# Kernel optimization log

Hardware: AMD Instinct MI355X
Metric: run time of the kernel (lower is better)

Reference implementation:

```python
import math
import jax, jax.numpy as jnp
import numpy as np

B, S, D, H, DH, R, V = 8, 1024, 1024, 8, 512, 36, 32002  # DH = d_model//2, HD = h*DH = 4096
HD = H * DH
LN_EPS = 1e-5


def setup_inputs() -> dict:
    key = jax.random.key(0)
    ks = jax.random.split(key, 16)

    def n(k, shp, std=0.02):
        return jax.random.normal(k, shp, jnp.float32) * std

    pre_words = jax.random.randint(ks[0], (B, S), 0, V)
    img_features = jax.random.normal(ks[1], (B, R, D), jnp.float32)
    exp_embed = n(ks[2], (V, D)).at[0].set(0.0)  # padding_idx=0
    # id2visual table: sparse nonneg rows over 36 regions; zero rows -> textual tokens
    id2vis = (jax.random.uniform(ks[3], (V, R)) < 0.05).astype(jnp.float32)
    # stacked params for 2 transformer layers; weights stored (in, out) so y = x @ W + b
    wq = n(ks[4], (2, D, HD)); bq = jnp.zeros((2, HD), jnp.float32)
    wk = n(ks[5], (2, D, HD)); bk = jnp.zeros((2, HD), jnp.float32)
    wv = n(ks[6], (2, D, HD)); bv = jnp.zeros((2, HD), jnp.float32)
    wo = n(ks[7], (2, HD, D)); bo = jnp.zeros((2, D), jnp.float32)
    w1 = n(ks[8], (2, D, D)); b1 = jnp.zeros((2, D), jnp.float32)
    w2 = n(ks[9], (2, D, D)); b2 = jnp.zeros((2, D), jnp.float32)
    ln1_g = jnp.ones((2, D), jnp.float32); ln1_b = jnp.zeros((2, D), jnp.float32)
    ln2_g = jnp.ones((2, D), jnp.float32); ln2_b = jnp.zeros((2, D), jnp.float32)
    return dict(pre_words=pre_words, img_features=img_features, exp_embed=exp_embed,
                id2vis=id2vis, wq=wq, bq=bq, wk=wk, bk=bk, wv=wv, bv=bv, wo=wo, bo=bo,
                w1=w1, b1=b1, w2=w2, b2=b2, ln1_g=ln1_g, ln1_b=ln1_b, ln2_g=ln2_g, ln2_b=ln2_b)


def _layer_norm(x, g, b):
    m = x.mean(-1, keepdims=True)
    v = ((x - m) ** 2).mean(-1, keepdims=True)
    return (x - m) / jnp.sqrt(v + LN_EPS) * g + b


def _softmax_one(x):
    # shifted-denominator softmax: exp(x - max) / (1 + sum exp(x - max))
    x = x - x.max(-1, keepdims=True)
    e = jnp.exp(x)
    return e / (1.0 + e.sum(-1, keepdims=True))


def reference(pre_words, img_features, exp_embed, id2vis, wq, bq, wk, bk, wv, bv,
              wo, bo, w1, b1, w2, b2, ln1_g, ln1_b, ln2_g, ln2_b):
    # token embedding: textual (masked to 0 where a visual row exists) + visual bmm
    te = exp_embed[pre_words]                       # (B,S,D)
    vids = id2vis[pre_words]                        # (B,S,R)
    word_mask = vids.sum(-1, keepdims=True) != 0    # (B,S,1)
    ve = jnp.einsum('bsr,brd->bsd', vids, img_features)
    x = jnp.where(word_mask, 0.0, te) + ve          # (B,S,D)

    scale = 1.0 / math.sqrt(DH)
    for i in range(2):  # two structurally identical transformer layers
        h = _layer_norm(x, ln1_g[i], ln1_b[i])
        q = (h @ wq[i] + bq[i]).reshape(B, S, H, DH).transpose(0, 2, 1, 3)
        k = (h @ wk[i] + bk[i]).reshape(B, S, H, DH).transpose(0, 2, 1, 3)
        v = (h @ wv[i] + bv[i]).reshape(B, S, H, DH).transpose(0, 2, 1, 3)
        attn = _softmax_one(jnp.einsum('bhqd,bhkd->bhqk', q, k) * scale)  # (B,H,S,S)
        o = jnp.einsum('bhqk,bhkd->bhqd', attn, v)
        o = o.transpose(0, 2, 1, 3).reshape(B, S, HD)
        x = x + (o @ wo[i] + bo[i])
        f = _layer_norm(x, ln2_g[i], ln2_b[i])
        f = jax.nn.gelu(f @ w1[i] + b1[i], approximate=False) @ w2[i] + b2[i]
        x = x + f
    return x
```

## Files before the change

### kernel.cpp

```cpp
#include <hip/hip_runtime.h>


using u16 = unsigned short;
typedef __attribute__((ext_vector_type(8))) short bf16x8;
typedef __attribute__((ext_vector_type(4))) float f32x4;

__device__ __forceinline__ float b2f(u16 u) {
  union { unsigned int i; float f; } v; v.i = ((unsigned int)u) << 16; return v.f;
}
__device__ __forceinline__ u16 f2b(float f) {
  union { float f; unsigned int i; } v; v.f = f;
  unsigned int i = v.i;
  return (u16)((i + 0x7FFFu + ((i >> 16) & 1u)) >> 16);
}
__device__ __forceinline__ float gelu_f(float x) {
  return 0.5f * x * (1.f + erff(x * 0.70710678118654752f));
}
__device__ __forceinline__ void async16(void* lds, const void* g) {
  __builtin_amdgcn_global_load_lds((const __attribute__((address_space(1))) void*)g,
                                   (__attribute__((address_space(3))) void*)lds, 16, 0, 0);
}
__device__ __forceinline__ void storeC(float* p, float v) { *p = v; }
__device__ __forceinline__ void storeC(u16* p, float v) { *p = f2b(v); }

__global__ __launch_bounds__(256) void embed_k(
    const int* __restrict__ words, const float* __restrict__ img,
    const float* __restrict__ emb, const float* __restrict__ id2v,
    float* __restrict__ x)
{
  __shared__ float vs[36];
  int tok = blockIdx.x, b = tok >> 10, t = threadIdx.x;
  int wd = words[tok];
  if (t < 36) vs[t] = id2v[(size_t)wd * 36 + t];
  __syncthreads();
  bool any = false;
#pragma unroll
  for (int r = 0; r < 36; ++r) any = any || (vs[r] != 0.f);
#pragma unroll
  for (int i = 0; i < 4; ++i) {
    int d = t + (i << 8);
    float acc = 0.f;
    for (int r = 0; r < 36; ++r) {
      float vv = vs[r];
      if (vv != 0.f) acc += vv * img[((size_t)(b * 36 + r) << 10) + d];
    }
    float te = any ? 0.f : emb[((size_t)wd << 10) + d];
    x[((size_t)tok << 10) + d] = te + acc;
  }
}

__global__ __launch_bounds__(256) void ln_k(
    const float* __restrict__ x, u16* __restrict__ out,
    const float* __restrict__ g, const float* __restrict__ bb)
{
  __shared__ float red[4];
  int row = blockIdx.x, t = threadIdx.x;
  const float* xr = x + ((size_t)row << 10);
  float v[4], s = 0.f;
#pragma unroll
  for (int i = 0; i < 4; ++i) { v[i] = xr[t + (i << 8)]; s += v[i]; }
#pragma unroll
  for (int o = 32; o; o >>= 1) s += __shfl_xor(s, o, 64);
  if ((t & 63) == 0) red[t >> 6] = s;
  __syncthreads();
  s = red[0] + red[1] + red[2] + red[3];
  float mean = s * 0.0009765625f;
  float q = 0.f;
#pragma unroll
  for (int i = 0; i < 4; ++i) { float d = v[i] - mean; q += d * d; }
  __syncthreads();
#pragma unroll
  for (int o = 32; o; o >>= 1) q += __shfl_xor(q, o, 64);
  if ((t & 63) == 0) red[t >> 6] = q;
  __syncthreads();
  q = red[0] + red[1] + red[2] + red[3];
  float rstd = rsqrtf(q * 0.0009765625f + 1e-5f);
  u16* orow = out + ((size_t)row << 10);
#pragma unroll
  for (int i = 0; i < 4; ++i) {
    int d = t + (i << 8);
    orow[d] = f2b((v[i] - mean) * rstd * g[d] + bb[d]);
  }
}

__global__ __launch_bounds__(256) void sm_k(const u16* __restrict__ S, u16* __restrict__ P)
{
  size_t row = ((size_t)blockIdx.x << 2) + (threadIdx.x >> 6);
  const int lane = threadIdx.x & 63;
  const u16* sr = S + (row << 10) + (lane << 4);
  ushort4 sv[4];
#pragma unroll
  for (int i = 0; i < 4; ++i) sv[i] = *(const ushort4*)(sr + (i << 2));
  float v[16];
#pragma unroll
  for (int i = 0; i < 4; ++i) {
    v[4 * i + 0] = b2f(sv[i].x); v[4 * i + 1] = b2f(sv[i].y);
    v[4 * i + 2] = b2f(sv[i].z); v[4 * i + 3] = b2f(sv[i].w);
  }
  float m = v[0];
#pragma unroll
  for (int i = 1; i < 16; ++i) m = fmaxf(m, v[i]);
#pragma unroll
  for (int o = 32; o; o >>= 1) m = fmaxf(m, __shfl_xor(m, o, 64));
  float s = 0.f;
#pragma unroll
  for (int i = 0; i < 16; ++i) { v[i] = __expf(v[i] - m); s += v[i]; }
#pragma unroll
  for (int o = 32; o; o >>= 1) s += __shfl_xor(s, o, 64);
  const float inv = 1.f / (1.f + s);
  u16* pr = P + (row << 10) + (lane << 4);
#pragma unroll
  for (int i = 0; i < 4; ++i) {
    ushort4 pv;
    pv.x = f2b(v[4 * i + 0] * inv); pv.y = f2b(v[4 * i + 1] * inv);
    pv.z = f2b(v[4 * i + 2] * inv); pv.w = f2b(v[4 * i + 3] * inv);
    *(ushort4*)(pr + (i << 2)) = pv;
  }
}

__global__ __launch_bounds__(256) void tr_k(
    const float* __restrict__ src, u16* __restrict__ dst, int ls, int ld)
{
  __shared__ u16 tile[64][65];
  int c0 = blockIdx.x << 6, r0 = blockIdx.y << 6;
  int tx = threadIdx.x & 63, ty0 = threadIdx.x >> 6;
#pragma unroll
  for (int i = 0; i < 16; ++i) {
    int ty = (ty0 << 4) + i;
    tile[ty][tx] = f2b(src[(size_t)(r0 + ty) * ls + (c0 + tx)]);
  }
  __syncthreads();
#pragma unroll
  for (int i = 0; i < 16; ++i) {
    int ty = (ty0 << 4) + i;
    dst[(size_t)(c0 + ty) * ld + (r0 + tx)] = tile[tx][ty];
  }
}

template <typename CT, int ACT, int BIAS, int RESID, int SPLIT>
__global__ __launch_bounds__(512, 1) void gemm8p(
    const u16* __restrict__ A, const u16* __restrict__ Bt,
    CT* __restrict__ C, const float* __restrict__ bias,
    const float* __restrict__ resid,
    int M, int N, int K, int lda, int ldb, int ldc, float scale,
    int zbase, int zdiv, int ga, int gb, int gc,
    long long aS1, long long aS2, long long bS1, long long bS2,
    long long cS1, long long cS2,
    const float* __restrict__ bias2, CT* __restrict__ C2)
{
  __shared__ u16 lA[2][256 * 64];
  __shared__ u16 lB[2][256 * 64];
  const int nwg = gridDim.x * gridDim.y;
  const int id = blockIdx.y * gridDim.x + blockIdx.x;
  const int qq = nwg >> 3, rr8 = nwg & 7;
  const int xcd = id & 7, off = id >> 3;
  const int swz = (xcd < rr8 ? xcd * (qq + 1) : rr8 * (qq + 1) + (xcd - rr8) * qq) + off;
  const int bx = swz % gridDim.x, by = swz / gridDim.x;

  long long lz = blockIdx.z;
  long long gz = zbase + lz;
  long long zA = ga ? gz : lz, zB = gb ? gz : lz, zC = gc ? gz : lz;
  size_t aOff = (size_t)((zA / zdiv) * aS1 + (zA % zdiv) * aS2);
  size_t bOff = (size_t)((zB / zdiv) * bS1 + (zB % zdiv) * bS2);
  size_t cOff = (size_t)((zC / zdiv) * cS1 + (zC % zdiv) * cS2);
  const int m0 = by << 8, n0 = bx << 8;
  const int tid = threadIdx.x, lane = tid & 63, w = tid >> 6;
  const int wm = w >> 2, wn = w & 3;
  const int srow8 = lane >> 3;
  const int schunk = (lane & 7) ^ srow8;
  const int fr = lane & 15, hi = lane >> 4;

  f32x4 acc[8][4];
#pragma unroll
  for (int mi = 0; mi < 8; ++mi)
#pragma unroll
    for (int ni = 0; ni < 4; ++ni) acc[mi][ni] = 0.f;

  const u16* Ab = A + aOff;
  const u16* Bb = Bt + bOff;

  auto ST_B = [&](int buf, int k0) {
#pragma unroll
    for (int s = 0; s < 4; ++s) {
      const int rb = (s << 6) + (w << 3);
      async16(&lB[buf][rb << 6], Bb + (size_t)(n0 + rb + srow8) * ldb + (k0 + (schunk << 3)));
    }
  };
  auto ST_A02 = [&](int buf, int k0) {
#pragma unroll
    for (int s = 0; s < 4; s += 2) {
      const int rb = (s << 6) + (w << 3);
      async16(&lA[buf][rb << 6], Ab + (size_t)(m0 + rb + srow8) * lda + (k0 + (schunk << 3)));
    }
  };
  auto ST_A13 = [&](int buf, int k0) {
#pragma unroll
    for (int s = 1; s < 4; s += 2) {
      const int rb = (s << 6) + (w << 3);
      async16(&lA[buf][rb << 6], Ab + (size_t)(m0 + rb + srow8) * lda + (k0 + (schunk << 3)));
    }
  };

  const int nt = K >> 6;
  ST_B(0, 0); ST_A02(0, 0); ST_A13(0, 0);
  ST_B(1, 64); ST_A02(1, 64);

  for (int t = 0; t < nt; ++t) {
    const int cur = t & 1;
    if (t + 1 < nt) asm volatile("s_waitcnt vmcnt(6)" ::: "memory");
    else            asm volatile("s_waitcnt vmcnt(0)" ::: "memory");
    __builtin_amdgcn_s_barrier();
    __builtin_amdgcn_sched_barrier(0);

    bf16x8 b8[4][2];
    const int kt2 = (t + 2) << 6;
#pragma unroll
    for (int p = 0; p < 4; ++p) {
      if (p == 0) {
#pragma unroll
        for (int ni = 0; ni < 4; ++ni)
#pragma unroll
          for (int ks = 0; ks < 2; ++ks) {
            const int R = (wn << 6) + (ni << 4) + fr;
            const int q = (ks << 2) + hi;
            b8[ni][ks] = *(const bf16x8*)&lB[cur][(R << 6) + ((q ^ (R & 7)) << 3)];
          }
      }
      bf16x8 a8[2][2];
#pragma unroll
      for (int i = 0; i < 2; ++i)
#pragma unroll
        for (int ks = 0; ks < 2; ++ks) {
          const int mi = (p << 1) + i;
          const int R = (wm << 7) + (mi << 4) + fr;
          const int q = (ks << 2) + hi;
          a8[i][ks] = *(const bf16x8*)&lA[cur][(R << 6) + ((q ^ (R & 7)) << 3)];
        }
      if (p == 0) { if (t + 1 < nt) ST_A13(cur ^ 1, (t + 1) << 6); }
      else if (p == 1) { if (t + 2 < nt) ST_B(cur, kt2); }
      else if (p == 2) { if (t + 2 < nt) ST_A02(cur, kt2); }
      __builtin_amdgcn_s_barrier();
      asm volatile("s_waitcnt lgkmcnt(0)" ::: "memory");
      __builtin_amdgcn_sched_barrier(0);
      __builtin_amdgcn_s_setprio(1);
#pragma unroll
      for (int i = 0; i < 2; ++i)
#pragma unroll
        for (int ni = 0; ni < 4; ++ni)
#pragma unroll
          for (int ks = 0; ks < 2; ++ks)
            acc[(p << 1) + i][ni] =
                __builtin_amdgcn_mfma_f32_16x16x32_bf16(a8[i][ks], b8[ni][ks],
                                                        acc[(p << 1) + i][ni], 0, 0, 0);
      __builtin_amdgcn_s_setprio(0);
      __builtin_amdgcn_s_barrier();
      __builtin_amdgcn_sched_barrier(0);
    }
  }

  const int r4 = hi << 2, cc = fr;
  const int half = N >> 1;
#pragma unroll
  for (int mi = 0; mi < 8; ++mi) {
#pragma unroll
    for (int ni = 0; ni < 4; ++ni) {
      const int col = n0 + (wn << 6) + (ni << 4) + cc;
      CT* Cd = C;
      int colx = col;
      const float* bp = bias;
      if (SPLIT && col >= half) { Cd = C2; colx = col - half; bp = bias2; }
      float bcol = 0.f;
      if (BIAS == 1) bcol = bp[colx];
#pragma unroll
      for (int j = 0; j < 4; ++j) {
        const int row = m0 + (wm << 7) + (mi << 4) + r4 + j;
        float v = acc[mi][ni][j] * scale + bcol;
        if (BIAS == 2) v += bias[row];
        if (ACT == 1) v = gelu_f(v);
        const size_t idx = cOff + (size_t)row * ldc + colx;
        if (RESID) v += resid[idx];
        storeC(&Cd[idx], v);
      }
    }
  }
}

template <typename CT, int ACT, int BIAS, int RESID, int BN>
__global__ __launch_bounds__(256, 4) void gemm_t(
    const u16* __restrict__ A, const u16* __restrict__ Bt,
    CT* __restrict__ C, const float* __restrict__ bias,
    const float* __restrict__ resid,
    int M, int N, int K, int lda, int ldb, int ldc, float scale,
    int zbase, int zdiv, int ga, int gb, int gc,
    long long aS1, long long aS2, long long bS1, long long bS2,
    long long cS1, long long cS2)
{
  constexpr int NACC = BN / 32;
  __shared__ u16 lA[128 * 64];
  __shared__ u16 lB[BN * 64];
  const int nwg = gridDim.x * gridDim.y;
  const int id = blockIdx.y * gridDim.x + blockIdx.x;
  const int qq = nwg >> 3, rr8 = nwg & 7;
  const int xcd = id & 7, off = id >> 3;
  const int swz = (xcd < rr8 ? xcd * (qq + 1) : rr8 * (qq + 1) + (xcd - rr8) * qq) + off;
  const int bx = swz % gridDim.x, by = swz / gridDim.x;

  long long lz = blockIdx.z;
  long long gz = zbase + lz;
  long long zA = ga ? gz : lz, zB = gb ? gz : lz, zC = gc ? gz : lz;
  size_t aOff = (size_t)((zA / zdiv) * aS1 + (zA % zdiv) * aS2);
  size_t bOff = (size_t)((zB / zdiv) * bS1 + (zB % zdiv) * bS2);
  size_t cOff = (size_t)((zC / zdiv) * cS1 + (zC % zdiv) * cS2);
  const int m0 = by << 7, n0 = bx * BN;
  const int tid = threadIdx.x, lane = tid & 63, w = tid >> 6;
  const int wm = w >> 1, wn = w & 1;
  const int srow8 = lane >> 3;
  const int schunk = (lane & 7) ^ srow8;
  const int fr = lane & 15, hi = lane >> 4;

  f32x4 acc[4][NACC];
#pragma unroll
  for (int mi = 0; mi < 4; ++mi)
#pragma unroll
    for (int ni = 0; ni < NACC; ++ni) acc[mi][ni] = 0.f;

  const u16* Ab = A + aOff;
  const u16* Bb = Bt + bOff;

  for (int k0 = 0; k0 < K; k0 += 64) {
#pragma unroll
    for (int s = 0; s < 4; ++s) {
      const int rb = (s << 5) + (w << 3);
      async16(&lA[rb << 6], Ab + (size_t)(m0 + rb + srow8) * lda + (k0 + (schunk << 3)));
    }
#pragma unroll
    for (int s = 0; s < BN / 32; ++s) {
      const int rb = (s << 5) + (w << 3);
      async16(&lB[rb << 6], Bb + (size_t)(n0 + rb + srow8) * ldb + (k0 + (schunk << 3)));
    }
    __syncthreads();
#pragma unroll
    for (int ks = 0; ks < 2; ++ks) {
      const int q = (ks << 2) + hi;
      bf16x8 a8[4], b8[NACC];
#pragma unroll
      for (int mi = 0; mi < 4; ++mi) {
        const int R = (wm << 6) + (mi << 4) + fr;
        a8[mi] = *(const bf16x8*)&lA[(R << 6) + ((q ^ (R & 7)) << 3)];
      }
#pragma unroll
      for (int ni = 0; ni < NACC; ++ni) {
        const int R = wn * (BN / 2) + (ni << 4) + fr;
        b8[ni] = *(const bf16x8*)&lB[(R << 6) + ((q ^ (R & 7)) << 3)];
      }
#pragma unroll
      for (int mi = 0; mi < 4; ++mi)
#pragma unroll
        for (int ni = 0; ni < NACC; ++ni)
          acc[mi][ni] = __builtin_amdgcn_mfma_f32_16x16x32_bf16(a8[mi], b8[ni], acc[mi][ni], 0, 0, 0);
    }
    __syncthreads();
  }

  const int r4 = hi << 2, cc = fr;
#pragma unroll
  for (int mi = 0; mi < 4; ++mi) {
#pragma unroll
    for (int ni = 0; ni < NACC; ++ni) {
      const int col = n0 + wn * (BN / 2) + (ni << 4) + cc;
      float bcol = 0.f;
      if (BIAS == 1) bcol = bias[col];
#pragma unroll
      for (int j = 0; j < 4; ++j) {
        const int row = m0 + (wm << 6) + (mi << 4) + r4 + j;
        float v = acc[mi][ni][j] * scale + bcol;
        if (BIAS == 2) v += bias[row];
        if (ACT == 1) v = gelu_f(v);
        const size_t idx = cOff + (size_t)row * ldc + col;
        if (RESID) v += resid[idx];
        storeC(&C[idx], v);
      }
    }
  }
}

extern "C" void kernel_launch(void* const* d_in, const int* in_sizes, int n_in,
                              void* d_out, int out_size, void* d_ws, size_t ws_size,
                              hipStream_t stream)
{
  (void)in_sizes; (void)n_in; (void)out_size;
  const int*   pre_words = (const int*)d_in[0];
  const float* img  = (const float*)d_in[1];
  const float* emb  = (const float*)d_in[2];
  const float* id2v = (const float*)d_in[3];
  const float* wq = (const float*)d_in[4];  const float* bq = (const float*)d_in[5];
  const float* wk = (const float*)d_in[6];  const float* bk = (const float*)d_in[7];
  const float* wv = (const float*)d_in[8];  const float* bv = (const float*)d_in[9];
  const float* wo = (const float*)d_in[10]; const float* bo = (const float*)d_in[11];
  const float* w1 = (const float*)d_in[12]; const float* b1 = (const float*)d_in[13];
  const float* w2 = (const float*)d_in[14]; const float* b2 = (const float*)d_in[15];
  const float* ln1g = (const float*)d_in[16]; const float* ln1b = (const float*)d_in[17];
  const float* ln2g = (const float*)d_in[18]; const float* ln2b = (const float*)d_in[19];

  const size_t FIXED = 88080384 + (size_t)(1 << 16);
  int g = 1;
  for (int c = 8; c >= 1; c >>= 1)
    if (FIXED + (size_t)c * 33554432 + 4194304 <= ws_size) { g = c; break; }
  int nc = 1;
  int ncmax = 8 * g > 64 ? 64 : 8 * g;
  for (int c = ncmax; c >= 1; c >>= 1)
    if (FIXED + (size_t)g * 33554432 + (size_t)c * 4194304 <= ws_size) { nc = c; break; }

  char* p = (char*)d_ws;
  auto alloc = [&](size_t bytes) -> void* {
    void* r = (void*)p; p += (bytes + 255) & ~(size_t)255; return r;
  };
  float* x  = (float*)alloc((size_t)8192 * 1024 * 4);
  u16* h    = (u16*)alloc((size_t)8192 * 1024 * 2);
  u16* Qg   = (u16*)alloc((size_t)g * 1024 * 4096 * 2);
  u16* Og   = (u16*)alloc((size_t)g * 1024 * 4096 * 2);
  u16* ff   = Qg;
  u16* Kg   = (u16*)alloc((size_t)g * 1024 * 4096 * 2);
  u16* Vtg  = (u16*)alloc((size_t)g * 4096 * 1024 * 2);
  u16* wqkt = (u16*)alloc((size_t)8192 * 1024 * 2);
  u16* wvt  = (u16*)alloc((size_t)4096 * 1024 * 2);
  u16* wot  = (u16*)alloc((size_t)1024 * 4096 * 2);
  u16* w1t  = (u16*)alloc((size_t)1024 * 1024 * 2);
  u16* w2t  = (u16*)alloc((size_t)1024 * 1024 * 2);
  u16* Sc   = (u16*)alloc((size_t)nc << 21);
  u16* Pp   = (u16*)alloc((size_t)nc << 21);

  embed_k<<<8192, 256, 0, stream>>>(pre_words, img, emb, id2v, x);

  const float qk_scale = 0.044194173824159216f;
  for (int L = 0; L < 2; ++L) {
    const float* WQ = wq + (size_t)L * 1024 * 4096;
    const float* WK = wk + (size_t)L * 1024 * 4096;
    const float* WV = wv + (size_t)L * 1024 * 4096;
    const float* WO = wo + (size_t)L * 4096 * 1024;
    const float* W1 = w1 + (size_t)L * 1024 * 1024;
    const float* W2 = w2 + (size_t)L * 1024 * 1024;

    tr_k<<<dim3(64, 16), 256, 0, stream>>>(WQ, wqkt, 4096, 1024);
    tr_k<<<dim3(64, 16), 256, 0, stream>>>(WK, wqkt + (size_t)4096 * 1024, 4096, 1024);
    tr_k<<<dim3(64, 16), 256, 0, stream>>>(WV, wvt, 4096, 1024);
    tr_k<<<dim3(16, 64), 256, 0, stream>>>(WO, wot, 1024, 4096);
    tr_k<<<dim3(16, 16), 256, 0, stream>>>(W1, w1t, 1024, 1024);
    tr_k<<<dim3(16, 16), 256, 0, stream>>>(W2, w2t, 1024, 1024);

    ln_k<<<8192, 256, 0, stream>>>(x, h, ln1g + L * 1024, ln1b + L * 1024);

    for (int g0 = 0; g0 < 8; g0 += g) {
      const u16* hg = h + (size_t)g0 * 1048576;
      const int Mg = 1024 * g;
      gemm8p<u16, 0, 1, 0, 1><<<dim3(32, Mg >> 8), 512, 0, stream>>>(
          hg, wqkt, Qg, bq + (size_t)L * 4096, nullptr,
          Mg, 8192, 1024, 1024, 1024, 4096, 1.f,
          0, 1, 0, 0, 0, 0, 0, 0, 0, 0, 0,
          bk + (size_t)L * 4096, Kg);
      gemm8p<u16, 0, 2, 0, 0><<<dim3(4, 16, g), 512, 0, stream>>>(
          wvt, h, Vtg, bv + (size_t)L * 4096, nullptr,
          4096, 1024, 1024, 1024, 1024, 1024, 1.f,
          g0, 1, 0, 1, 0, 0, 0, 1048576LL, 0, 4194304LL, 0,
          nullptr, nullptr);
      for (int c0 = 0; c0 < 8 * g; c0 += nc) {
        gemm8p<u16, 0, 0, 0, 0><<<dim3(4, 4, nc), 512, 0, stream>>>(
            Qg, Kg, Sc, nullptr, nullptr,
            1024, 1024, 512, 4096, 4096, 1024, qk_scale,
            c0, 8, 1, 1, 0,
            4194304LL, 512LL, 4194304LL, 512LL, 8388608LL, 1048576LL,
            nullptr, nullptr);
        sm_k<<<nc << 8, 256, 0, stream>>>(Sc, Pp);
        gemm8p<u16, 0, 0, 0, 0><<<dim3(2, 4, nc), 512, 0, stream>>>(
            Pp, Vtg, Og, nullptr, nullptr,
            1024, 512, 1024, 1024, 1024, 4096, 1.f,
            c0, 8, 0, 1, 1,
            8388608LL, 1048576LL, 4194304LL, 524288LL, 4194304LL, 512LL,
            nullptr, nullptr);
      }
      gemm_t<float, 0, 1, 1, 64><<<dim3(16, Mg >> 7), 256, 0, stream>>>(
          Og, wot, x + (size_t)g0 * 1048576, bo + (size_t)L * 1024,
          x + (size_t)g0 * 1048576,
          Mg, 1024, 4096, 4096, 4096, 1024, 1.f,
          0, 1, 0, 0, 0, 0, 0, 0, 0, 0, 0);
    }

    ln_k<<<8192, 256, 0, stream>>>(x, h, ln2g + L * 1024, ln2b + L * 1024);

    gemm_t<u16, 1, 1, 0, 64><<<dim3(16, 64), 256, 0, stream>>>(
        h, w1t, ff, b1 + (size_t)L * 1024, nullptr,
        8192, 1024, 1024, 1024, 1024, 1024, 1.f,
        0, 1, 0, 0, 0, 0, 0, 0, 0, 0, 0);
    float* cdst = (L == 1) ? (float*)d_out : x;
    gemm_t<float, 0, 1, 1, 64><<<dim3(16, 64), 256, 0, stream>>>(
        ff, w2t, cdst, b2 + (size_t)L * 1024, x,
        8192, 1024, 1024, 1024, 1024, 1024, 1.f,
        0, 1, 0, 0, 0, 0, 0, 0, 0, 0, 0);
  }
}
```

Before: 1.500 ms.

## Replace gemm_t with double-buffered 128x256 GEMM, alias buffers to shrink workspace

Replaces the simple single-buffered 128x64 GEMM used for the output projection and the FFN with a 512-thread, 128x256-tile kernel. The new kernel double-buffers LDS with async loads and raises MFMA priority while computing. Softmax now writes in place into the score buffer and the attention output aliases Q, which frees workspace so larger head groups or chunks fit. It also drops the sched_barriers in the existing 8-wave kernel. Larger tiles mean fewer workgroups for the N=1024 GEMMs, so occupancy and tail balance may suffer. The in-place and aliased buffers depend on Q not being read after the PV GEMM writes into it.

```diff
diff --git a/kernel.cpp b/kernel.cpp
--- a/kernel.cpp
+++ b/kernel.cpp
@@ -210,7 +210,6 @@
     if (t + 1 < nt) asm volatile("s_waitcnt vmcnt(6)" ::: "memory");
     else            asm volatile("s_waitcnt vmcnt(0)" ::: "memory");
     __builtin_amdgcn_s_barrier();
-    __builtin_amdgcn_sched_barrier(0);
 
     bf16x8 b8[4][2];
     const int kt2 = (t + 2) << 6;
@@ -254,7 +253,6 @@
                                                         acc[(p << 1) + i][ni], 0, 0, 0);
       __builtin_amdgcn_s_setprio(0);
       __builtin_amdgcn_s_barrier();
-      __builtin_amdgcn_sched_barrier(0);
     }
   }
 
@@ -285,19 +283,15 @@
   }
 }
 
-template <typename CT, int ACT, int BIAS, int RESID, int BN>
-__global__ __launch_bounds__(256, 4) void gemm_t(
+template <typename CT, int ACT, int BIAS, int RESID>
+__global__ __launch_bounds__(512, 1) void gemm8pn(
     const u16* __restrict__ A, const u16* __restrict__ Bt,
     CT* __restrict__ C, const float* __restrict__ bias,
     const float* __restrict__ resid,
-    int M, int N, int K, int lda, int ldb, int ldc, float scale,
-    int zbase, int zdiv, int ga, int gb, int gc,
-    long long aS1, long long aS2, long long bS1, long long bS2,
-    long long cS1, long long cS2)
-{
-  constexpr int NACC = BN / 32;
-  __shared__ u16 lA[128 * 64];
-  __shared__ u16 lB[BN * 64];
+    int M, int N, int K, int lda, int ldb, int ldc, float scale)
+{
+  __shared__ u16 lA[2][128 * 64];
+  __shared__ u16 lB[2][256 * 64];
   const int nwg = gridDim.x * gridDim.y;
   const int id = blockIdx.y * gridDim.x + blockIdx.x;
   const int qq = nwg >> 3, rr8 = nwg & 7;
@@ -305,78 +299,90 @@
   const int swz = (xcd < rr8 ? xcd * (qq + 1) : rr8 * (qq + 1) + (xcd - rr8) * qq) + off;
   const int bx = swz % gridDim.x, by = swz / gridDim.x;
 
-  long long lz = blockIdx.z;
-  long long gz = zbase + lz;
-  long long zA = ga ? gz : lz, zB = gb ? gz : lz, zC = gc ? gz : lz;
-  size_t aOff = (size_t)((zA / zdiv) * aS1 + (zA % zdiv) * aS2);
-  size_t bOff = (size_t)((zB / zdiv) * bS1 + (zB % zdiv) * bS2);
-  size_t cOff = (size_t)((zC / zdiv) * cS1 + (zC % zdiv) * cS2);
-  const int m0 = by << 7, n0 = bx * BN;
+  const int m0 = by << 7, n0 = bx << 8;
   const int tid = threadIdx.x, lane = tid & 63, w = tid >> 6;
-  const int wm = w >> 1, wn = w & 1;
+  const int wm = w >> 2, wn = w & 3;
   const int srow8 = lane >> 3;
   const int schunk = (lane & 7) ^ srow8;
   const int fr = lane & 15, hi = lane >> 4;
 
-  f32x4 acc[4][NACC];
+  f32x4 acc[4][4];
 #pragma unroll
   for (int mi = 0; mi < 4; ++mi)
 #pragma unroll
-    for (int ni = 0; ni < NACC; ++ni) acc[mi][ni] = 0.f;
-
-  const u16* Ab = A + aOff;
-  const u16* Bb = Bt + bOff;
-
-  for (int k0 = 0; k0 < K; k0 += 64) {
+    for (int ni = 0; ni < 4; ++ni) acc[mi][ni] = 0.f;
+
+  auto ST = [&](int buf, int k0) {
+#pragma unroll
+    for (int s = 0; s < 2; ++s) {
+      const int rb = (s << 6) + (w << 3);
+      async16(&lA[buf][rb << 6], A + (size_t)(m0 + rb + srow8) * lda + (k0 + (schunk << 3)));
+    }
 #pragma unroll
     for (int s = 0; s < 4; ++s) {
-      const int rb = (s << 5) + (w << 3);
-      async16(&lA[rb << 6], Ab + (size_t)(m0 + rb + srow8) * lda + (k0 + (schunk << 3)));
-    }
-#pragma unroll
-    for (int s = 0; s < BN / 32; ++s) {
-      const int rb = (s << 5) + (w << 3);
-      async16(&lB[rb << 6], Bb + (size_t)(n0 + rb + srow8) * ldb + (k0 + (schunk << 3)));
-    }
-    __syncthreads();
-#pragma unroll
-    for (int ks = 0; ks < 2; ++ks) {
-      const int q = (ks << 2) + hi;
-      bf16x8 a8[4], b8[NACC];
-#pragma unroll
-      for (int mi = 0; mi < 4; ++mi) {
+      const int rb = (s << 6) + (w << 3);
+      async16(&lB[buf][rb << 6], Bt + (size_t)(n0 + rb + srow8) * ldb + (k0 + (schunk << 3)));
+    }
+  };
+
+  const int nt = K >> 6;
+  ST(0, 0);
+  ST(1, 64);
+  for (int t = 0; t < nt; ++t) {
+    const int cur = t & 1;
+    if (t + 1 < nt) asm volatile("s_waitcnt vmcnt(6)" ::: "memory");
+    else            asm volatile("s_waitcnt vmcnt(0)" ::: "memory");
+    __builtin_amdgcn_s_barrier();
+
+    bf16x8 a8[4][2], b8[4][2];
+#pragma unroll
+    for (int mi = 0; mi < 4; ++mi)
+#pragma unroll
+      for (int ks = 0; ks < 2; ++ks) {
         const int R = (wm << 6) + (mi << 4) + fr;
-        a8[mi] = *(const bf16x8*)&lA[(R << 6) + ((q ^ (R & 7)) << 3)];
+        const int q = (ks << 2) + hi;
+        a8[mi][ks] = *(const bf16x8*)&lA[cur][(R << 6) + ((q ^ (R & 7)) << 3)];
       }
 #pragma unroll
-      for (int ni = 0; ni < NACC; ++ni) {
-        const int R = wn * (BN / 2) + (ni << 4) + fr;
-        b8[ni] = *(const bf16x8*)&lB[(R << 6) + ((q ^ (R & 7)) << 3)];
+    for (int ni = 0; ni < 4; ++ni)
+#pragma unroll
+      for (int ks = 0; ks < 2; ++ks) {
+        const int R = (wn << 6) + (ni << 4) + fr;
+        const int q = (ks << 2) + hi;
+        b8[ni][ks] = *(const bf16x8*)&lB[cur][(R << 6) + ((q ^ (R & 7)) << 3)];
       }
-#pragma unroll
-      for (int mi = 0; mi < 4; ++mi)
-#pragma unroll
-        for (int ni = 0; ni < NACC; ++ni)
-          acc[mi][ni] = __builtin_amdgcn_mfma_f32_16x16x32_bf16(a8[mi], b8[ni], acc[mi][ni], 0, 0, 0);
-    }
-    __syncthreads();
+    asm volatile("s_waitcnt lgkmcnt(0)" ::: "memory");
+    __builtin_amdgcn_sched_barrier(0);
+    __builtin_amdgcn_s_setprio(1);
+#pragma unroll
+    for (int mi = 0; mi < 4; ++mi)
+#pragma unroll
+      for (int ni = 0; ni < 4; ++ni)
+#pragma unroll
+        for (int ks = 0; ks < 2; ++ks)
+          acc[mi][ni] = __builtin_amdgcn_mfma_f32_16x16x32_bf16(a8[mi][ks], b8[ni][ks],
+                                                               acc[mi][ni], 0, 0, 0);
+    __builtin_amdgcn_s_setprio(0);
+    if (t + 2 < nt) {
+      __builtin_amdgcn_s_barrier();
+      ST(cur, (t + 2) << 6);
+    }
   }
 
   const int r4 = hi << 2, cc = fr;
 #pragma unroll
   for (int mi = 0; mi < 4; ++mi) {
 #pragma unroll
-    for (int ni = 0; ni < NACC; ++ni) {
-      const int col = n0 + wn * (BN / 2) + (ni << 4) + cc;
+    for (int ni = 0; ni < 4; ++ni) {
+      const int col = n0 + (wn << 6) + (ni << 4) + cc;
       float bcol = 0.f;
       if (BIAS == 1) bcol = bias[col];
 #pragma unroll
       for (int j = 0; j < 4; ++j) {
         const int row = m0 + (wm << 6) + (mi << 4) + r4 + j;
         float v = acc[mi][ni][j] * scale + bcol;
-        if (BIAS == 2) v += bias[row];
         if (ACT == 1) v = gelu_f(v);
-        const size_t idx = cOff + (size_t)row * ldc + col;
+        const size_t idx = (size_t)row * ldc + col;
         if (RESID) v += resid[idx];
         storeC(&C[idx], v);
       }
@@ -405,11 +411,11 @@
   const size_t FIXED = 88080384 + (size_t)(1 << 16);
   int g = 1;
   for (int c = 8; c >= 1; c >>= 1)
-    if (FIXED + (size_t)c * 33554432 + 4194304 <= ws_size) { g = c; break; }
+    if (FIXED + (size_t)c * 25165824 + 2097152 <= ws_size) { g = c; break; }
   int nc = 1;
   int ncmax = 8 * g > 64 ? 64 : 8 * g;
   for (int c = ncmax; c >= 1; c >>= 1)
-    if (FIXED + (size_t)g * 33554432 + (size_t)c * 4194304 <= ws_size) { nc = c; break; }
+    if (FIXED + (size_t)g * 25165824 + (size_t)c * 2097152 <= ws_size) { nc = c; break; }
 
   char* p = (char*)d_ws;
   auto alloc = [&](size_t bytes) -> void* {
@@ -418,7 +424,7 @@
   float* x  = (float*)alloc((size_t)8192 * 1024 * 4);
   u16* h    = (u16*)alloc((size_t)8192 * 1024 * 2);
   u16* Qg   = (u16*)alloc((size_t)g * 1024 * 4096 * 2);
-  u16* Og   = (u16*)alloc((size_t)g * 1024 * 4096 * 2);
+  u16* Og   = Qg;
   u16* ff   = Qg;
   u16* Kg   = (u16*)alloc((size_t)g * 1024 * 4096 * 2);
   u16* Vtg  = (u16*)alloc((size_t)g * 4096 * 1024 * 2);
@@ -428,7 +434,6 @@
   u16* w1t  = (u16*)alloc((size_t)1024 * 1024 * 2);
   u16* w2t  = (u16*)alloc((size_t)1024 * 1024 * 2);
   u16* Sc   = (u16*)alloc((size_t)nc << 21);
-  u16* Pp   = (u16*)alloc((size_t)nc << 21);
 
   embed_k<<<8192, 256, 0, stream>>>(pre_words, img, emb, id2v, x);
 
@@ -470,31 +475,28 @@
             c0, 8, 1, 1, 0,
             4194304LL, 512LL, 4194304LL, 512LL, 8388608LL, 1048576LL,
             nullptr, nullptr);
-        sm_k<<<nc << 8, 256, 0, stream>>>(Sc, Pp);
+        sm_k<<<nc << 8, 256, 0, stream>>>(Sc, Sc);
         gemm8p<u16, 0, 0, 0, 0><<<dim3(2, 4, nc), 512, 0, stream>>>(
-            Pp, Vtg, Og, nullptr, nullptr,
+            Sc, Vtg, Og, nullptr, nullptr,
             1024, 512, 1024, 1024, 1024, 4096, 1.f,
             c0, 8, 0, 1, 1,
             8388608LL, 1048576LL, 4194304LL, 524288LL, 4194304LL, 512LL,
             nullptr, nullptr);
       }
-      gemm_t<float, 0, 1, 1, 64><<<dim3(16, Mg >> 7), 256, 0, stream>>>(
+      gemm8pn<float, 0, 1, 1><<<dim3(4, Mg >> 7), 512, 0, stream>>>(
           Og, wot, x + (size_t)g0 * 1048576, bo + (size_t)L * 1024,
           x + (size_t)g0 * 1048576,
-          Mg, 1024, 4096, 4096, 4096, 1024, 1.f,
-          0, 1, 0, 0, 0, 0, 0, 0, 0, 0, 0);
+          Mg, 1024, 4096, 4096, 4096, 1024, 1.f);
     }
 
     ln_k<<<8192, 256, 0, stream>>>(x, h, ln2g + L * 1024, ln2b + L * 1024);
 
-    gemm_t<u16, 1, 1, 0, 64><<<dim3(16, 64), 256, 0, stream>>>(
+    gemm8pn<u16, 1, 1, 0><<<dim3(4, 64), 512, 0, stream>>>(
         h, w1t, ff, b1 + (size_t)L * 1024, nullptr,
-        8192, 1024, 1024, 1024, 1024, 1024, 1.f,
-        0, 1, 0, 0, 0, 0, 0, 0, 0, 0, 0);
+        8192, 1024, 1024, 1024, 1024, 1024, 1.f);
     float* cdst = (L == 1) ? (float*)d_out : x;
-    gemm_t<float, 0, 1, 1, 64><<<dim3(16, 64), 256, 0, stream>>>(
+    gemm8pn<float, 0, 1, 1><<<dim3(4, 64), 512, 0, stream>>>(
         ff, w2t, cdst, b2 + (size_t)L * 1024, x,
-        8192, 1024, 1024, 1024, 1024, 1024, 1.f,
-        0, 1, 0, 0, 0, 0, 0, 0, 0, 0, 0);
-  }
-}
+        8192, 1024, 1024, 1024, 1024, 1024, 1.f);
+  }
+}
```

Measured after the change: 1.497 ms. Within noise of the previous version (-0.1%).
